# Performance work log

Measured on AMD Instinct MI355X. Metric: run time of the kernel, lower is better.

Reference implementation:

```python
import jax, jax.numpy as jnp
import numpy as np

# --- dimensions (match init_kwargs) ---
T, B = 64, 8            # time steps, batch
H, I, O, G = 512, 256, 8, 4   # hidden, input, output, attention groups
GS = I // G              # group size = 64 (equal groups)
E_H = int(0.8 * H)       # 409 excitatory hidden units
ZC = round(0.2 * H)      # 102 zeroed columns for h2o / attn masks
DT = 0.02
AX = DT / 0.1            # alpha_x = 0.2
AW = DT / 1.0            # alpha_w = 0.02

# --- static EI masks (constants of the architecture) ---
_sign_h = np.concatenate([np.ones(E_H), -np.ones(H - E_H)]).astype(np.float32)  # [H]
_m_h2h = np.tile(_sign_h, (H, 1)); np.fill_diagonal(_m_h2h, 0.0)                 # remove_diag
_exist = np.concatenate([np.ones(H - ZC), np.zeros(ZC)]).astype(np.float32)     # [H]
_m_attn = np.tile(_sign_h * _exist, (G, 1))   # attn: e_prop=0.8, zero_cols_prop=0.2
_m_h2o = np.tile(_exist, (O, 1))              # h2o: e_prop=1 (all +), zero last ZC cols
MASK_H2H = jnp.asarray(_m_h2h)
MASK_ATTN = jnp.asarray(_m_attn)
MASK_H2O = jnp.asarray(_m_h2o)


def setup_inputs() -> dict:
    key = jax.random.key(0)
    ks = jax.random.split(key, 8)
    x = jax.random.normal(ks[0], (T, B, I), dtype=jnp.float32)
    Rs = jax.random.uniform(ks[1], (T, B, 1), dtype=jnp.float32)
    # EILinear init: uniform(0, sqrt(1/(in - zero_cols))) * init_gain
    W_x2h = jax.random.uniform(ks[2], (H, I), dtype=jnp.float32, maxval=np.sqrt(1.0 / I)) * 0.5
    W_h2h = jax.random.uniform(ks[3], (H, H), dtype=jnp.float32, maxval=np.sqrt(1.0 / H))
    b_h2h = jnp.zeros((H,), jnp.float32)
    W_h2o = jax.random.uniform(ks[4], (O, H), dtype=jnp.float32, maxval=np.sqrt(1.0 / (H - ZC))) * 0.5
    W_attn = jax.random.uniform(ks[5], (G, H), dtype=jnp.float32, maxval=np.sqrt(1.0 / (H - ZC)))
    b_attn = jnp.zeros((G,), jnp.float32)
    kappa = jnp.full((6,), AW, dtype=jnp.float32)  # kappa_w init = alpha_w
    return {"x": x, "Rs": Rs, "W_x2h": W_x2h, "W_h2h": W_h2h, "b_h2h": b_h2h,
            "W_h2o": W_h2o, "W_attn": W_attn, "b_attn": b_attn, "kappa": kappa}


def reference(x, Rs, W_x2h, W_h2h, b_h2h, W_h2o, W_attn, b_attn, kappa):
    relu = jax.nn.relu
    Wx_pos = relu(W_x2h)                 # x2h mask is all ones (e_prop=1)
    Wh_pos = relu(W_h2h)
    eff_attn = relu(W_attn) * MASK_ATTN  # [G, H]
    Wx_floor = jax.lax.stop_gradient(Wx_pos)  # clamp bound (.detach())
    Wh_floor = jax.lax.stop_gradient(Wh_pos)

    def step(carry, inp):
        state, out, wx, wh = carry       # [B,H],[B,H],[B,H,I],[B,H,H]
        xt, Rt = inp                     # [B,I], [B,1]
        # attention gating over input groups
        aw = jax.nn.softmax(out @ eff_attn.T + b_attn, axis=-1)   # [B,G]
        af = jnp.repeat(aw, GS, axis=-1)                          # [B,I]
        xin = relu(xt) * af * G                                   # sigma_in = 0
        # plastic effective weights: (relu(W) + w) * mask
        eff_x = Wx_pos[None] + wx                                 # [B,H,I] (mask = ones)
        eff_h = (Wh_pos[None] + wh) * MASK_H2H[None]              # [B,H,H]
        total = (jnp.einsum('bhi,bi->bh', eff_x, xin)
                 + jnp.einsum('bhj,bj->bh', eff_h, out) + b_h2h)
        new_state = state * (1.0 - AX) + total * AX               # sigma_rec = 0
        new_out = jnp.tanh(relu(new_state))                       # retanh
        # Hebbian fast-weight updates (sigma_w = 0)
        R = Rt[:, :, None]                                        # [B,1,1]
        wx2 = wx * (1.0 - AW) + DT * R * (
            kappa[0] * xin[:, None, :]
            + kappa[1] * new_out[:, :, None]
            + kappa[2] * new_out[:, :, None] * xin[:, None, :])
        wx2 = jnp.maximum(wx2, -Wx_floor[None])
        wh2 = wh * (1.0 - AW) + DT * R * (
            kappa[3] * out[:, None, :]
            + kappa[4] * new_out[:, :, None]
            + kappa[5] * new_out[:, :, None] * out[:, None, :])
        wh2 = jnp.maximum(wh2, -Wh_floor[None])
        return (new_state, new_out, wx2, wh2), new_out

    init = (jnp.zeros((B, H), x.dtype), jnp.zeros((B, H), x.dtype),
            jnp.zeros((B, H, I), x.dtype), jnp.zeros((B, H, H), x.dtype))
    _, hs = jax.lax.scan(step, init, (x, Rs))                      # hs: [T,B,H]
    os = jnp.einsum('tbh,oh->tbo', hs, relu(W_h2o) * MASK_H2O)     # [T,B,O]
    return os, hs
```

## Files before the change

### kernel.cpp

```cpp
#include <hip/hip_runtime.h>

#define T_N 64
#define B_N 8
#define H_N 512
#define I_N 256
#define O_N 8
#define G_N 4

constexpr float DT_ = 0.02f;
constexpr float AX_ = 0.2f;
constexpr float AW_ = 0.02f;

__device__ __forceinline__ float ldf_agent(const float* p) {
    return __hip_atomic_load(p, __ATOMIC_RELAXED, __HIP_MEMORY_SCOPE_AGENT);
}
__device__ __forceinline__ void stf_agent(float* p, float v) {
    __hip_atomic_store(p, v, __ATOMIC_RELAXED, __HIP_MEMORY_SCOPE_AGENT);
}
__device__ __forceinline__ unsigned ldu_agent(const unsigned* p) {
    return __hip_atomic_load(p, __ATOMIC_RELAXED, __HIP_MEMORY_SCOPE_AGENT);
}

__global__ __launch_bounds__(1024) void rnn_scan(
    const float* __restrict__ x, const float* __restrict__ Rs,
    const float* __restrict__ W_x2h, const float* __restrict__ W_h2h,
    const float* __restrict__ b_h2h, const float* __restrict__ W_h2o,
    const float* __restrict__ W_attn, const float* __restrict__ b_attn,
    const float* __restrict__ kappa, float* __restrict__ d_out,
    unsigned* __restrict__ barrier_cnt)
{
    float* os = d_out;
    float* hs = d_out + T_N * B_N * O_N;

    const int tid  = threadIdx.x;
    const int wid  = tid >> 6;
    const int lane = tid & 63;
    const int bk   = blockIdx.x;
    const int b    = bk & 7;
    const int hg   = bk >> 3;
    const int h    = (hg << 4) | wid;

    float ea[G_N][8];
#pragma unroll
    for (int g = 0; g < G_N; ++g)
#pragma unroll
        for (int c = 0; c < 8; ++c) {
            int j = lane + 64 * c;
            float w = fmaxf(W_attn[g * H_N + j], 0.0f);
            float m = (j < 409) ? 1.0f : ((j < 410) ? -1.0f : 0.0f);
            ea[g][c] = w * m;
        }

    float Wxp[4], wx[4];
#pragma unroll
    for (int c = 0; c < 4; ++c) {
        Wxp[c] = fmaxf(W_x2h[h * I_N + lane + 64 * c], 0.0f);
        wx[c]  = 0.0f;
    }
    float Whp[8], wh[8], msk[8];
#pragma unroll
    for (int c = 0; c < 8; ++c) {
        int j = lane + 64 * c;
        Whp[c] = fmaxf(W_h2h[h * H_N + j], 0.0f);
        wh[c]  = 0.0f;
        float m = (j <= 408) ? 1.0f : -1.0f;
        msk[c] = (j == h) ? 0.0f : m;
    }
    const float bh = b_h2h[h];
    const float k0 = kappa[0], k1 = kappa[1], k2 = kappa[2];
    const float k3 = kappa[3], k4 = kappa[4], k5 = kappa[5];
    const float ba0 = b_attn[0], ba1 = b_attn[1], ba2 = b_attn[2], ba3 = b_attn[3];

    float state = 0.0f;
    unsigned* cnt = barrier_cnt + b * 32;

    float xv[4];
#pragma unroll
    for (int c = 0; c < 4; ++c) xv[c] = fmaxf(x[(size_t)b * I_N + lane + 64 * c], 0.0f);
    float Rcur = Rs[b];

    for (int t = 0; t < T_N; ++t) {
        float outp[8];
        if (t == 0) {
#pragma unroll
            for (int c = 0; c < 8; ++c) outp[c] = 0.0f;
        } else {
            const float* hrow = hs + ((size_t)(t - 1) * B_N + b) * H_N;
#pragma unroll
            for (int c = 0; c < 8; ++c) outp[c] = ldf_agent(hrow + lane + 64 * c);
        }

        float red[9];
#pragma unroll
        for (int g = 0; g < G_N; ++g) {
            float l = 0.0f;
#pragma unroll
            for (int c = 0; c < 8; ++c) l = fmaf(outp[c], ea[g][c], l);
            red[g] = l;
        }
#pragma unroll
        for (int c = 0; c < 4; ++c)
            red[4 + c] = (Wxp[c] + wx[c]) * xv[c];
        {
            float a = 0.0f;
#pragma unroll
            for (int c = 0; c < 8; ++c) a = fmaf((Whp[c] + wh[c]) * msk[c], outp[c], a);
            red[8] = a;
        }
#pragma unroll
        for (int off = 32; off >= 1; off >>= 1) {
#pragma unroll
            for (int k = 0; k < 9; ++k) red[k] += __shfl_xor(red[k], off, 64);
        }

        float l0 = red[0] + ba0, l1 = red[1] + ba1;
        float l2 = red[2] + ba2, l3 = red[3] + ba3;
        float mx = fmaxf(fmaxf(l0, l1), fmaxf(l2, l3));
        float e0 = expf(l0 - mx), e1 = expf(l1 - mx);
        float e2 = expf(l2 - mx), e3 = expf(l3 - mx);
        float inv = 4.0f / (e0 + e1 + e2 + e3);
        float aw0 = e0 * inv, aw1 = e1 * inv, aw2 = e2 * inv, aw3 = e3 * inv;

        float total = red[4] * aw0 + red[5] * aw1 + red[6] * aw2 + red[7] * aw3
                    + red[8] + bh;

        state = state * (1.0f - AX_) + total * AX_;
        float ns = fmaxf(state, 0.0f);
        float no = tanhf(ns);

        if (lane == 0) stf_agent(&hs[((size_t)t * B_N + b) * H_N + h], no);
        __syncthreads();
        if (tid == 0)
            __hip_atomic_fetch_add(cnt, 1u, __ATOMIC_RELAXED, __HIP_MEMORY_SCOPE_AGENT);

        float xin[4];
#pragma unroll
        for (int c = 0; c < 4; ++c) xin[c] = xv[c] * ((c == 0) ? aw0 : (c == 1) ? aw1 : (c == 2) ? aw2 : aw3);
        float dr = DT_ * Rcur;
#pragma unroll
        for (int c = 0; c < 4; ++c) {
            float hebb = fmaf(k2 * no, xin[c], fmaf(k0, xin[c], k1 * no));
            wx[c] = fmaxf(fmaf(wx[c], 1.0f - AW_, dr * hebb), -Wxp[c]);
        }
#pragma unroll
        for (int c = 0; c < 8; ++c) {
            float hebb = fmaf(k5 * no, outp[c], fmaf(k3, outp[c], k4 * no));
            wh[c] = fmaxf(fmaf(wh[c], 1.0f - AW_, dr * hebb), -Whp[c]);
        }

        float xvn[4] = {0.f, 0.f, 0.f, 0.f};
        float Rn = 0.0f;
        if (t + 1 < T_N) {
            const float* xr = x + ((size_t)(t + 1) * B_N + b) * I_N;
#pragma unroll
            for (int c = 0; c < 4; ++c) xvn[c] = xr[lane + 64 * c];
            Rn = Rs[(t + 1) * B_N + b];
        }

        if (tid == 0) {
            unsigned target = 32u * (unsigned)(t + 1);
            while (ldu_agent(cnt) < target) __builtin_amdgcn_s_sleep(1);
        }
        __syncthreads();

#pragma unroll
        for (int c = 0; c < 4; ++c) xv[c] = fmaxf(xvn[c], 0.0f);
        Rcur = Rn;
    }

    {
        int v = (hg << 4) | wid;
        int t = v >> 3;
        int o = v & 7;
        const float* hrow = hs + ((size_t)t * B_N + b) * H_N;
        float acc = 0.0f;
#pragma unroll
        for (int c = 0; c < 8; ++c) {
            int j = lane + 64 * c;
            float w = fmaxf(W_h2o[o * H_N + j], 0.0f);
            if (j >= 410) w = 0.0f;
            acc = fmaf(ldf_agent(hrow + j), w, acc);
        }
#pragma unroll
        for (int off = 32; off >= 1; off >>= 1) acc += __shfl_xor(acc, off, 64);
        if (lane == 0) os[t * (B_N * O_N) + b * O_N + o] = acc;
    }
}

extern "C" void kernel_launch(void* const* d_in, const int* in_sizes, int n_in,
                              void* d_out, int out_size, void* d_ws, size_t ws_size,
                              hipStream_t stream) {
    (void)in_sizes; (void)n_in; (void)out_size; (void)ws_size;
    const float* x      = (const float*)d_in[0];
    const float* Rs     = (const float*)d_in[1];
    const float* W_x2h  = (const float*)d_in[2];
    const float* W_h2h  = (const float*)d_in[3];
    const float* b_h2h  = (const float*)d_in[4];
    const float* W_h2o  = (const float*)d_in[5];
    const float* W_attn = (const float*)d_in[6];
    const float* b_attn = (const float*)d_in[7];
    const float* kappa  = (const float*)d_in[8];
    float* out = (float*)d_out;
    unsigned* cnt = (unsigned*)d_ws;

    hipMemsetAsync(d_ws, 0, B_N * 32 * sizeof(unsigned), stream);
    rnn_scan<<<dim3(256), dim3(1024), 0, stream>>>(
        x, Rs, W_x2h, W_h2h, b_h2h, W_h2o, W_attn, b_attn, kappa, out, cnt);
}
```

Before: 264.1 us.

## Replace per-step counter barrier with tagged 64-bit flag-value exchange

Each hidden unit now publishes its new output packed with a step tag into a double-buffered 64-bit exchange array. One wave per block polls until every tag matches, then broadcasts the values through shared memory. This removes the per-step atomic counter barrier and its separate reload of hs. Softmax exp and tanh are also swapped for fast intrinsics. The costs are heavier polling traffic (8 loads per lane per spin), an extra workspace memset, and slightly lower tanh and exp accuracy.

```diff
diff --git a/kernel.cpp b/kernel.cpp
--- a/kernel.cpp
+++ b/kernel.cpp
@@ -11,14 +11,27 @@
 constexpr float AX_ = 0.2f;
 constexpr float AW_ = 0.02f;
 
+using u64 = unsigned long long;
+
 __device__ __forceinline__ float ldf_agent(const float* p) {
     return __hip_atomic_load(p, __ATOMIC_RELAXED, __HIP_MEMORY_SCOPE_AGENT);
 }
 __device__ __forceinline__ void stf_agent(float* p, float v) {
     __hip_atomic_store(p, v, __ATOMIC_RELAXED, __HIP_MEMORY_SCOPE_AGENT);
 }
+__device__ __forceinline__ u64 ld64_agent(const u64* p) {
+    return __hip_atomic_load(p, __ATOMIC_RELAXED, __HIP_MEMORY_SCOPE_AGENT);
+}
+__device__ __forceinline__ void st64_agent(u64* p, u64 v) {
+    __hip_atomic_store(p, v, __ATOMIC_RELAXED, __HIP_MEMORY_SCOPE_AGENT);
+}
 __device__ __forceinline__ unsigned ldu_agent(const unsigned* p) {
     return __hip_atomic_load(p, __ATOMIC_RELAXED, __HIP_MEMORY_SCOPE_AGENT);
+}
+
+__device__ __forceinline__ float fast_tanh_pos(float x) {
+    float ex = __expf(2.0f * x);
+    return 1.0f - 2.0f / (ex + 1.0f);
 }
 
 __global__ __launch_bounds__(1024) void rnn_scan(
@@ -27,10 +40,12 @@
     const float* __restrict__ b_h2h, const float* __restrict__ W_h2o,
     const float* __restrict__ W_attn, const float* __restrict__ b_attn,
     const float* __restrict__ kappa, float* __restrict__ d_out,
-    unsigned* __restrict__ barrier_cnt)
+    u64* __restrict__ comm, unsigned* __restrict__ barrier_cnt)
 {
     float* os = d_out;
     float* hs = d_out + T_N * B_N * O_N;
+
+    __shared__ float s_out[H_N];
 
     const int tid  = threadIdx.x;
     const int wid  = tid >> 6;
@@ -72,24 +87,17 @@
     const float ba0 = b_attn[0], ba1 = b_attn[1], ba2 = b_attn[2], ba3 = b_attn[3];
 
     float state = 0.0f;
-    unsigned* cnt = barrier_cnt + b * 32;
 
     float xv[4];
 #pragma unroll
     for (int c = 0; c < 4; ++c) xv[c] = fmaxf(x[(size_t)b * I_N + lane + 64 * c], 0.0f);
     float Rcur = Rs[b];
 
+    float outp[8];
+#pragma unroll
+    for (int c = 0; c < 8; ++c) outp[c] = 0.0f;
+
     for (int t = 0; t < T_N; ++t) {
-        float outp[8];
-        if (t == 0) {
-#pragma unroll
-            for (int c = 0; c < 8; ++c) outp[c] = 0.0f;
-        } else {
-            const float* hrow = hs + ((size_t)(t - 1) * B_N + b) * H_N;
-#pragma unroll
-            for (int c = 0; c < 8; ++c) outp[c] = ldf_agent(hrow + lane + 64 * c);
-        }
-
         float red[9];
 #pragma unroll
         for (int g = 0; g < G_N; ++g) {
@@ -116,8 +124,8 @@
         float l0 = red[0] + ba0, l1 = red[1] + ba1;
         float l2 = red[2] + ba2, l3 = red[3] + ba3;
         float mx = fmaxf(fmaxf(l0, l1), fmaxf(l2, l3));
-        float e0 = expf(l0 - mx), e1 = expf(l1 - mx);
-        float e2 = expf(l2 - mx), e3 = expf(l3 - mx);
+        float e0 = __expf(l0 - mx), e1 = __expf(l1 - mx);
+        float e2 = __expf(l2 - mx), e3 = __expf(l3 - mx);
         float inv = 4.0f / (e0 + e1 + e2 + e3);
         float aw0 = e0 * inv, aw1 = e1 * inv, aw2 = e2 * inv, aw3 = e3 * inv;
 
@@ -126,16 +134,16 @@
 
         state = state * (1.0f - AX_) + total * AX_;
         float ns = fmaxf(state, 0.0f);
-        float no = tanhf(ns);
-
-        if (lane == 0) stf_agent(&hs[((size_t)t * B_N + b) * H_N + h], no);
-        __syncthreads();
-        if (tid == 0)
-            __hip_atomic_fetch_add(cnt, 1u, __ATOMIC_RELAXED, __HIP_MEMORY_SCOPE_AGENT);
-
-        float xin[4];
-#pragma unroll
-        for (int c = 0; c < 4; ++c) xin[c] = xv[c] * ((c == 0) ? aw0 : (c == 1) ? aw1 : (c == 2) ? aw2 : aw3);
+        float no = fast_tanh_pos(ns);
+
+        if (lane == 0) {
+            union { float f; unsigned u; } cv; cv.f = no;
+            u64 pk = ((u64)(unsigned)(t + 1) << 32) | (u64)cv.u;
+            st64_agent(&comm[((size_t)(t & 1) * B_N + b) * H_N + h], pk);
+            stf_agent(&hs[((size_t)t * B_N + b) * H_N + h], no);
+        }
+
+        float xin[4] = { xv[0] * aw0, xv[1] * aw1, xv[2] * aw2, xv[3] * aw3 };
         float dr = DT_ * Rcur;
 #pragma unroll
         for (int c = 0; c < 4; ++c) {
@@ -148,25 +156,49 @@
             wh[c] = fmaxf(fmaf(wh[c], 1.0f - AW_, dr * hebb), -Whp[c]);
         }
 
-        float xvn[4] = {0.f, 0.f, 0.f, 0.f};
-        float Rn = 0.0f;
         if (t + 1 < T_N) {
             const float* xr = x + ((size_t)(t + 1) * B_N + b) * I_N;
+            float xvn[4];
 #pragma unroll
             for (int c = 0; c < 4; ++c) xvn[c] = xr[lane + 64 * c];
-            Rn = Rs[(t + 1) * B_N + b];
-        }
-
-        if (tid == 0) {
-            unsigned target = 32u * (unsigned)(t + 1);
-            while (ldu_agent(cnt) < target) __builtin_amdgcn_s_sleep(1);
-        }
-        __syncthreads();
-
-#pragma unroll
-        for (int c = 0; c < 4; ++c) xv[c] = fmaxf(xvn[c], 0.0f);
-        Rcur = Rn;
-    }
+            float Rn = Rs[(t + 1) * B_N + b];
+
+            if (wid == 0) {
+                const u64* crow = comm + ((size_t)(t & 1) * B_N + b) * H_N;
+                const unsigned want = (unsigned)(t + 1);
+                u64 pk[8];
+                bool ok;
+                do {
+                    ok = true;
+#pragma unroll
+                    for (int c = 0; c < 8; ++c) pk[c] = ld64_agent(crow + lane + 64 * c);
+#pragma unroll
+                    for (int c = 0; c < 8; ++c) ok &= ((unsigned)(pk[c] >> 32) == want);
+                } while (!__all(ok));
+#pragma unroll
+                for (int c = 0; c < 8; ++c) {
+                    union { unsigned u; float f; } cv; cv.u = (unsigned)pk[c];
+                    s_out[lane + 64 * c] = cv.f;
+                }
+            }
+            __syncthreads();
+#pragma unroll
+            for (int c = 0; c < 8; ++c) outp[c] = s_out[lane + 64 * c];
+            __syncthreads();
+
+#pragma unroll
+            for (int c = 0; c < 4; ++c) xv[c] = fmaxf(xvn[c], 0.0f);
+            Rcur = Rn;
+        }
+    }
+
+    unsigned* cnt = barrier_cnt + b * 32;
+    __syncthreads();
+    if (tid == 0) {
+        __hip_atomic_fetch_add(cnt, 1u, __ATOMIC_RELAXED, __HIP_MEMORY_SCOPE_AGENT);
+        while (ldu_agent(cnt) < 32u) __builtin_amdgcn_s_sleep(2);
+    }
+    __syncthreads();
 
     {
         int v = (hg << 4) | wid;
@@ -201,9 +233,11 @@
     const float* b_attn = (const float*)d_in[7];
     const float* kappa  = (const float*)d_in[8];
     float* out = (float*)d_out;
-    unsigned* cnt = (unsigned*)d_ws;
-
-    hipMemsetAsync(d_ws, 0, B_N * 32 * sizeof(unsigned), stream);
+
+    u64* comm     = (u64*)d_ws;
+    unsigned* cnt = (unsigned*)((char*)d_ws + 2 * B_N * H_N * 8);
+
+    hipMemsetAsync(d_ws, 0, 2 * B_N * H_N * 8 + B_N * 32 * 4, stream);
     rnn_scan<<<dim3(256), dim3(1024), 0, stream>>>(
-        x, Rs, W_x2h, W_h2h, b_h2h, W_h2o, W_attn, b_attn, kappa, out, cnt);
-}
+        x, Rs, W_x2h, W_h2h, b_h2h, W_h2o, W_attn, b_attn, kappa, out, comm, cnt);
+}
```

Measured after the change: 347.8 us. +31.7%, slower.
